# Optimization experiments

Hardware: AMD Instinct MI355X
Metric: run time of the kernel (lower is better)

Reference implementation:

```python
import jax, jax.numpy as jnp
import numpy as np

N_CORES = 64
N_QUBITS = 1024
QEMB = 256
N_EDGES = 448
BATCH = 512
NN_DIMS = (256, 512, 512, 256)


def setup_inputs() -> dict:
    key = jax.random.key(0)
    ks = jax.random.split(key, 12)
    inp = {
        "core_allocs": jax.random.randint(ks[0], (BATCH, N_QUBITS), 0, N_CORES, dtype=jnp.int32),
        "qubit_embs": jax.random.normal(ks[1], (N_QUBITS, QEMB), dtype=jnp.float32),
        "dummy_qubit_emb": jax.random.normal(ks[2], (QEMB,), dtype=jnp.float32),
        "edge_index": jax.random.randint(ks[3], (2, N_EDGES), 0, N_CORES, dtype=jnp.int32),
        "edge_weight": jax.random.uniform(ks[4], (N_EDGES,), dtype=jnp.float32),
        "W1": jax.random.normal(ks[5], (NN_DIMS[0], NN_DIMS[1]), dtype=jnp.float32) * 0.05,
        "b1": jax.random.normal(ks[6], (NN_DIMS[1],), dtype=jnp.float32) * 0.05,
        "W2": jax.random.normal(ks[7], (NN_DIMS[1], NN_DIMS[2]), dtype=jnp.float32) * 0.05,
        "b2": jax.random.normal(ks[8], (NN_DIMS[2],), dtype=jnp.float32) * 0.05,
        "W3": jax.random.normal(ks[9], (NN_DIMS[2], NN_DIMS[3]), dtype=jnp.float32) * 0.05,
        "b3": jax.random.normal(ks[10], (NN_DIMS[3],), dtype=jnp.float32) * 0.05,
    }
    return inp


def _gcn_norm(edge_index, edge_weight):
    # PyG gcn_norm: add self loops (weight 1), symmetric D^{-1/2} A D^{-1/2}.
    self_idx = jnp.arange(N_CORES, dtype=edge_index.dtype)
    row = jnp.concatenate([edge_index[0], self_idx])
    col = jnp.concatenate([edge_index[1], self_idx])
    w = jnp.concatenate([edge_weight, jnp.ones((N_CORES,), edge_weight.dtype)])
    deg = jax.ops.segment_sum(w, col, num_segments=N_CORES)  # degree at targets
    dinv = jnp.where(deg > 0, deg ** -0.5, 0.0)
    norm = dinv[row] * w * dinv[col]
    return row, col, norm


def reference(core_allocs, qubit_embs, dummy_qubit_emb, edge_index, edge_weight,
              W1, b1, W2, b2, W3, b3):
    # ---- unmixedCoreEmbs, vectorized: per-core max over assigned qubit embs,
    # dummy emb always included (cores never at capacity) ----
    def pool(alloc):  # alloc: [n_qubits] -> [n_cores, qemb]
        seg = jax.ops.segment_max(qubit_embs, alloc, num_segments=N_CORES)
        return jnp.maximum(seg, dummy_qubit_emb)  # also fixes -inf empty cores

    x = jax.vmap(pool)(core_allocs)  # [B, n_cores, qemb]

    # ---- GCNConv stack (same graph replicated per batch element) ----
    row, col, norm = _gcn_norm(edge_index, edge_weight)

    def gcn_layer(h, W, b):
        hw = h @ W  # [B, C, d_out]
        msg = hw[:, row, :] * norm[None, :, None]  # gather sources, scale
        agg = jnp.zeros((h.shape[0], N_CORES, W.shape[1]), hw.dtype).at[:, col, :].add(msg)
        return jax.nn.relu(agg + b)

    x = gcn_layer(x, W1, b1)
    x = gcn_layer(x, W2, b2)
    x = gcn_layer(x, W3, b3)
    return x  # [B, n_cores, nn_dims[-1]] (original returns this split per batch element)
```

## Files before the change

kernel.cpp:

```cpp
#include <hip/hip_runtime.h>
#include <type_traits>

typedef __attribute__((ext_vector_type(8))) short short8;
typedef __attribute__((ext_vector_type(4))) short short4v;
typedef __attribute__((ext_vector_type(4))) float f32x4;
typedef unsigned short u16;
typedef unsigned int u32;

#define N_EDGES 448

#define WS_ADJA 0
#define WS_ADJB 4096
#define WS_W1   8192
#define WS_W2   139264
#define WS_W3   401408
#define WS_DUM  532480
#define WS_B1   (WS_DUM + 256)
#define WS_B2   (WS_DUM + 768)
#define WS_B3   (WS_DUM + 1280)
#define WS_QE   534528

__device__ __forceinline__ float bf2f(u16 v) {
    u32 u = ((u32)v) << 16;
    return __builtin_bit_cast(float, u);
}
__device__ __forceinline__ u16 f2bf(float f) {
    u32 u = __builtin_bit_cast(u32, f);
    u32 r = u + 0x7FFFu + ((u >> 16) & 1u);
    return (u16)(r >> 16);
}
__device__ __forceinline__ float ldf(const void* p, int idx, u32 isf32) {
    return isf32 ? ((const float*)p)[idx] : bf2f(((const u16*)p)[idx]);
}

__global__ __launch_bounds__(512) void prep(
    const int* __restrict__ eidx, const void* __restrict__ ew,
    const void* __restrict__ qembs, const void* __restrict__ dummy,
    const void* __restrict__ W1, const void* __restrict__ b1,
    const void* __restrict__ W2, const void* __restrict__ b2,
    const void* __restrict__ W3, const void* __restrict__ b3,
    u16* __restrict__ ws) {
    const int t = threadIdx.x, bb = blockIdx.x;
    __shared__ u32 s_isf;
    if (t < 64) {
        const u16* qs = (const u16*)qembs;
        int c = 0;
#pragma unroll
        for (int j = 0; j < 4; j++) {
            u16 v = qs[(t * 4 + j) * 2];
            u32 e = (v >> 7) & 0xFF;
            c += (e >= 100 && e <= 134) ? 1 : 0;
        }
#pragma unroll
        for (int off = 32; off > 0; off >>= 1) c += __shfl_down(c, off, 64);
        if (t == 0) s_isf = (c < 128) ? 1u : 0u;
    }
    __syncthreads();
    const u32 isf32 = s_isf;

    if (t < 128) {
        const int bw = bb * 2 + (t >> 6);
        const int tl = t & 63;
        const void* src;
        int N, K32, dst, nt, kk;
        if (bw < 256)      { src = W1; N = 512; K32 = 8;  dst = WS_W1; nt = bw / 8;          kk = bw % 8; }
        else if (bw < 768) { src = W2; N = 512; K32 = 16; dst = WS_W2; nt = (bw - 256) / 16; kk = (bw - 256) % 16; }
        else               { src = W3; N = 256; K32 = 16; dst = WS_W3; nt = (bw - 768) / 16; kk = (bw - 768) % 16; }
        const int col = nt * 16 + (tl & 15);
        const int krow = kk * 32 + (tl >> 4) * 8;
        u16 v[8];
#pragma unroll
        for (int j = 0; j < 8; j++) v[j] = f2bf(ldf(src, (krow + j) * N + col, isf32));
        u16* o = ws + dst + (nt * K32 + kk) * 512 + tl * 8;
#pragma unroll
        for (int j = 0; j < 8; j++) o[j] = v[j];
    }
    if (t >= 256) {
        const int base = bb * 512 + (t - 256) * 2;
        ws[WS_QE + base]     = f2bf(ldf(qembs, base, isf32));
        ws[WS_QE + base + 1] = f2bf(ldf(qembs, base + 1, isf32));
    }
    if (bb == 1) {
#pragma unroll
        for (int j = 0; j < 4; j++) {
            int i = t + j * 512;
            if (i < 1792) {
                float v;
                if (i < 256)       v = ldf(dummy, i, isf32);
                else if (i < 768)  v = ldf(b1, i - 256, isf32);
                else if (i < 1280) v = ldf(b2, i - 768, isf32);
                else               v = ldf(b3, i - 1280, isf32);
                ws[WS_DUM + i] = f2bf(v);
            }
        }
    }
    if (bb == 0) {
        __shared__ float A[4096];
        __shared__ float deg[64];
        __shared__ float dinv[64];
        __shared__ int er[N_EDGES];
        __shared__ int ec[N_EDGES];
        __shared__ float ewf[N_EDGES];
        if (t < N_EDGES) {
            er[t] = eidx[t];
            ec[t] = eidx[N_EDGES + t];
            ewf[t] = ldf(ew, t, isf32);
        }
        if (t < 64) deg[t] = 1.0f;
        for (int i = t; i < 4096; i += 512) A[i] = 0.f;
        __syncthreads();
        if (t < N_EDGES) atomicAdd(&deg[ec[t]], ewf[t]);
        __syncthreads();
        if (t < 64) dinv[t] = 1.0f / sqrtf(deg[t]);
        __syncthreads();
        if (t < N_EDGES) atomicAdd(&A[ec[t] * 64 + er[t]], dinv[er[t]] * ewf[t] * dinv[ec[t]]);
        __syncthreads();
        if (t < 64) A[t * 64 + t] += dinv[t] * dinv[t];
        __syncthreads();
        for (int i = t; i < 4096; i += 512) {
            int chunk = i >> 9, m = (i >> 3) & 63, j = i & 7;
            ws[WS_ADJA + i] = f2bf(A[m * 64 + chunk * 8 + j]);
        }
        for (int i = t; i < 4096; i += 512) {
            int chunk = i >> 9, l = (i >> 3) & 63, j = i & 7;
            int ntc = chunk >> 1, kk = chunk & 1;
            int k = kk * 32 + (l >> 4) * 8 + j;
            int c2 = ntc * 16 + (l & 15);
            ws[WS_ADJB + i] = f2bf(A[c2 * 64 + k]);
        }
    }
}

__global__ __launch_bounds__(1024, 4) void fused(
    const int* __restrict__ allocs, const void* __restrict__ qembs,
    const u16* __restrict__ ws, void* __restrict__ out) {

    __shared__ __align__(16) u16 H[64 * 512];
    __shared__ u32 s_isf;

    const int t = threadIdx.x, bb = blockIdx.x;
    const int wave = t >> 6, lane = t & 63, quad = lane >> 4, nl = lane & 15;

    if (t < 64) {
        const u16* qs = (const u16*)qembs;
        int c = 0;
#pragma unroll
        for (int j = 0; j < 4; j++) {
            u16 v = qs[(t * 4 + j) * 2];
            u32 e = (v >> 7) & 0xFF;
            c += (e >= 100 && e <= 134) ? 1 : 0;
        }
#pragma unroll
        for (int off = 32; off > 0; off >>= 1) c += __shfl_down(c, off, 64);
        if (t == 0) s_isf = (c < 128) ? 1u : 0u;
    }
    __syncthreads();
    const u32 isf32 = s_isf;

    {
        int* LIST = (int*)H + 8192;
        int* CNT  = LIST + 1024;
        int* SST  = CNT + 64;
        int* WOF  = SST + 64;
        if (t < 64) CNT[t] = 0;
        __syncthreads();
        const int myc = allocs[bb * 1024 + t];
        atomicAdd(&CNT[myc], 1);
        __syncthreads();
        if (t < 64) {
            int v = CNT[t], s = v;
#pragma unroll
            for (int off = 1; off < 64; off <<= 1) {
                int u = __shfl_up(s, off, 64);
                if (t >= off) s += u;
            }
            SST[t] = s - v;
            WOF[t] = s - v;
        }
        __syncthreads();
        {
            int pos = atomicAdd(&WOF[myc], 1);
            LIST[pos] = t;
        }
        __syncthreads();
        float dums[4];
#pragma unroll
        for (int jj = 0; jj < 4; jj++) dums[jj] = bf2f(ws[WS_DUM + lane * 4 + jj]);
        const u16* wsq = ws + WS_QE;
        for (int i = 0; i < 4; i++) {
            const int c = wave * 4 + i;
            const int L = CNT[c], S = SST[c];
            float vm0 = -3.4e38f, vm1 = -3.4e38f, vm2 = -3.4e38f, vm3 = -3.4e38f;
            for (int j = 0; j < L; j++) {
                int q = LIST[S + j];
                uint2 r = *(const uint2*)(wsq + q * 256 + lane * 4);
                vm0 = fmaxf(vm0, bf2f((u16)(r.x & 0xffff)));
                vm1 = fmaxf(vm1, bf2f((u16)(r.x >> 16)));
                vm2 = fmaxf(vm2, bf2f((u16)(r.y & 0xffff)));
                vm3 = fmaxf(vm3, bf2f((u16)(r.y >> 16)));
            }
            short4v p;
            p[0] = (short)f2bf(fmaxf(vm0, dums[0]));
            p[1] = (short)f2bf(fmaxf(vm1, dums[1]));
            p[2] = (short)f2bf(fmaxf(vm2, dums[2]));
            p[3] = (short)f2bf(fmaxf(vm3, dums[3]));
            *(short4v*)(H + (lane >> 1) * 512 + c * 8 + (lane & 1) * 4) = p;
        }
    }
    __syncthreads();

    auto layerT = [&](auto K32c, const u16* __restrict__ W, const u16* __restrict__ bias) {
        constexpr int K32 = decltype(K32c)::value;
        const int s0 = wave * 2;
        u16* scr = H + (wave * 4 + 2) * 512;
        f32x4 acc[2][4];
#pragma unroll
        for (int s = 0; s < 2; s++)
#pragma unroll
            for (int rt = 0; rt < 4; rt++) acc[s][rt] = f32x4{0.f, 0.f, 0.f, 0.f};
#pragma unroll
        for (int kk = 0; kk < K32; kk++) {
            short8 a[4], bch[2];
#pragma unroll
            for (int rt = 0; rt < 4; rt++)
                a[rt] = *(const short8*)(H + (kk * 4 + quad) * 512 + (rt * 16 + nl) * 8);
#pragma unroll
            for (int s = 0; s < 2; s++)
                bch[s] = *(const short8*)(W + ((s0 + s) * K32 + kk) * 512 + lane * 8);
#pragma unroll
            for (int s = 0; s < 2; s++)
#pragma unroll
                for (int rt = 0; rt < 4; rt++)
                    acc[s][rt] = __builtin_amdgcn_mfma_f32_16x16x32_bf16(a[rt], bch[s], acc[s][rt], 0, 0, 0);
        }
        __syncthreads();
#pragma unroll
        for (int s = 0; s < 2; s++) {
            const int nt = s0 + s;
            f32x4 agg[4];
#pragma unroll
            for (int ntc = 0; ntc < 4; ntc++) agg[ntc] = f32x4{0.f, 0.f, 0.f, 0.f};
#pragma unroll
            for (int h = 0; h < 2; h++) {
#pragma unroll
                for (int r2 = 0; r2 < 2; r2++) {
                    f32x4 v = acc[s][2 * h + r2];
                    short4v p;
#pragma unroll
                    for (int rr = 0; rr < 4; rr++) p[rr] = (short)f2bf(v[rr]);
                    *(short4v*)(scr + nl * 40 + r2 * 16 + quad * 4) = p;
                }
                short8 hwf = *(const short8*)(scr + nl * 40 + quad * 8);
#pragma unroll
                for (int ntc = 0; ntc < 4; ntc++) {
                    short8 adjB = *(const short8*)(ws + WS_ADJB + (ntc * 2 + h) * 512 + lane * 8);
                    agg[ntc] = __builtin_amdgcn_mfma_f32_16x16x32_bf16(hwf, adjB, agg[ntc], 0, 0, 0);
                }
            }
            float bv[4];
#pragma unroll
            for (int rr = 0; rr < 4; rr++) bv[rr] = bf2f(bias[nt * 16 + quad * 4 + rr]);
#pragma unroll
            for (int ntc = 0; ntc < 4; ntc++) {
                short4v p;
#pragma unroll
                for (int rr = 0; rr < 4; rr++)
                    p[rr] = (short)f2bf(fmaxf(agg[ntc][rr] + bv[rr], 0.f));
                *(short4v*)(H + (nt * 2 + (quad >> 1)) * 512 + (ntc * 16 + nl) * 8 + (quad & 1) * 4) = p;
            }
        }
        __syncthreads();
    };

    auto layer3 = [&](const u16* __restrict__ W) {
        const int nt = wave;
        u16* scr = H + 16384 + wave * 640;
        f32x4 acc[4];
#pragma unroll
        for (int rt = 0; rt < 4; rt++) acc[rt] = f32x4{0.f, 0.f, 0.f, 0.f};
#pragma unroll
        for (int kk = 0; kk < 16; kk++) {
            short8 a[4];
#pragma unroll
            for (int rt = 0; rt < 4; rt++)
                a[rt] = *(const short8*)(H + (kk * 4 + quad) * 512 + (rt * 16 + nl) * 8);
            short8 bch = *(const short8*)(W + (nt * 16 + kk) * 512 + lane * 8);
#pragma unroll
            for (int rt = 0; rt < 4; rt++)
                acc[rt] = __builtin_amdgcn_mfma_f32_16x16x32_bf16(a[rt], bch, acc[rt], 0, 0, 0);
        }
        __syncthreads();
#pragma unroll
        for (int h = 0; h < 2; h++) {
#pragma unroll
            for (int r2 = 0; r2 < 2; r2++) {
                f32x4 v = acc[2 * h + r2];
                short4v p;
#pragma unroll
                for (int rr = 0; rr < 4; rr++) p[rr] = (short)f2bf(v[rr]);
                *(short4v*)(scr + nl * 40 + r2 * 16 + quad * 4) = p;
            }
            short8 hwf = *(const short8*)(scr + nl * 40 + quad * 8);
            *(short8*)(H + (nt * 2 + h) * 512 + lane * 8) = hwf;
        }
        __syncthreads();
    };

    auto finalOut = [&]() {
        const int rt2 = wave & 3, nt0 = (wave >> 2) * 4;
        short8 aA[2];
#pragma unroll
        for (int h = 0; h < 2; h++)
            aA[h] = *(const short8*)(ws + WS_ADJA + (h * 4 + quad) * 512 + (rt2 * 16 + nl) * 8);
        float* outf = (float*)out + (size_t)bb * 16384;
        u16* outu = (u16*)out + (size_t)bb * 16384;
#pragma unroll
        for (int ni = 0; ni < 4; ni++) {
            const int nt = nt0 + ni;
            short8 b0v = *(const short8*)(H + (nt * 2 + 0) * 512 + lane * 8);
            short8 b1v = *(const short8*)(H + (nt * 2 + 1) * 512 + lane * 8);
            f32x4 acc = f32x4{0.f, 0.f, 0.f, 0.f};
            acc = __builtin_amdgcn_mfma_f32_16x16x32_bf16(aA[0], b0v, acc, 0, 0, 0);
            acc = __builtin_amdgcn_mfma_f32_16x16x32_bf16(aA[1], b1v, acc, 0, 0, 0);
            const int n = nt * 16 + nl;
            const float bv = bf2f(ws[WS_B3 + n]);
#pragma unroll
            for (int rr = 0; rr < 4; rr++) {
                const int m2 = rt2 * 16 + quad * 4 + rr;
                float val = fmaxf(acc[rr] + bv, 0.f);
                if (isf32) outf[m2 * 256 + n] = val;
                else       outu[m2 * 256 + n] = f2bf(val);
            }
        }
    };

    layerT(std::integral_constant<int, 8>{},  ws + WS_W1, ws + WS_B1);
    layerT(std::integral_constant<int, 16>{}, ws + WS_W2, ws + WS_B2);
    layer3(ws + WS_W3);
    finalOut();
}

extern "C" void kernel_launch(void* const* d_in, const int* in_sizes, int n_in,
                              void* d_out, int out_size, void* d_ws, size_t ws_size,
                              hipStream_t stream) {
    const int* allocs = (const int*)d_in[0];
    const void* qembs = d_in[1];
    const void* dummy = d_in[2];
    const int* eidx   = (const int*)d_in[3];
    const void* ew    = d_in[4];
    const void* W1 = d_in[5];
    const void* b1 = d_in[6];
    const void* W2 = d_in[7];
    const void* b2 = d_in[8];
    const void* W3 = d_in[9];
    const void* b3 = d_in[10];
    u16* ws = (u16*)d_ws;

    prep<<<512, 512, 0, stream>>>(eidx, ew, qembs, dummy, W1, b1, W2, b2, W3, b3, ws);
    fused<<<512, 1024, 0, stream>>>(allocs, qembs, ws, d_out);
}
```

Before: 149.8 us.

## Stage final output through LDS for coalesced stores and widen pooling loads

```diff
diff --git a/kernel.cpp b/kernel.cpp
--- a/kernel.cpp
+++ b/kernel.cpp
@@ -19,6 +19,7 @@
 #define WS_B2   (WS_DUM + 768)
 #define WS_B3   (WS_DUM + 1280)
 #define WS_QE   534528
+#define WS_FLAG 796672
 
 __device__ __forceinline__ float bf2f(u16 v) {
     u32 u = ((u32)v) << 16;
@@ -128,34 +129,18 @@
             int c2 = ntc * 16 + (l & 15);
             ws[WS_ADJB + i] = f2bf(A[c2 * 64 + k]);
         }
-    }
-}
-
-__global__ __launch_bounds__(1024, 4) void fused(
-    const int* __restrict__ allocs, const void* __restrict__ qembs,
-    const u16* __restrict__ ws, void* __restrict__ out) {
+        if (t == 0) *(u32*)(ws + WS_FLAG) = isf32;
+    }
+}
+
+__global__ __launch_bounds__(1024, 8) void fused(
+    const int* __restrict__ allocs, const u16* __restrict__ ws,
+    void* __restrict__ out) {
 
     __shared__ __align__(16) u16 H[64 * 512];
-    __shared__ u32 s_isf;
 
     const int t = threadIdx.x, bb = blockIdx.x;
     const int wave = t >> 6, lane = t & 63, quad = lane >> 4, nl = lane & 15;
-
-    if (t < 64) {
-        const u16* qs = (const u16*)qembs;
-        int c = 0;
-#pragma unroll
-        for (int j = 0; j < 4; j++) {
-            u16 v = qs[(t * 4 + j) * 2];
-            u32 e = (v >> 7) & 0xFF;
-            c += (e >= 100 && e <= 134) ? 1 : 0;
-        }
-#pragma unroll
-        for (int off = 32; off > 0; off >>= 1) c += __shfl_down(c, off, 64);
-        if (t == 0) s_isf = (c < 128) ? 1u : 0u;
-    }
-    __syncthreads();
-    const u32 isf32 = s_isf;
 
     {
         int* LIST = (int*)H + 8192;
@@ -183,28 +168,33 @@
             LIST[pos] = t;
         }
         __syncthreads();
-        float dums[4];
-#pragma unroll
-        for (int jj = 0; jj < 4; jj++) dums[jj] = bf2f(ws[WS_DUM + lane * 4 + jj]);
+        const int half = lane >> 5, sl = lane & 31;
         const u16* wsq = ws + WS_QE;
         for (int i = 0; i < 4; i++) {
             const int c = wave * 4 + i;
             const int L = CNT[c], S = SST[c];
-            float vm0 = -3.4e38f, vm1 = -3.4e38f, vm2 = -3.4e38f, vm3 = -3.4e38f;
-            for (int j = 0; j < L; j++) {
+            float vm[8];
+#pragma unroll
+            for (int k = 0; k < 8; k++) vm[k] = bf2f(ws[WS_DUM + sl * 8 + k]);
+            for (int j = half; j < L; j += 2) {
                 int q = LIST[S + j];
-                uint2 r = *(const uint2*)(wsq + q * 256 + lane * 4);
-                vm0 = fmaxf(vm0, bf2f((u16)(r.x & 0xffff)));
-                vm1 = fmaxf(vm1, bf2f((u16)(r.x >> 16)));
-                vm2 = fmaxf(vm2, bf2f((u16)(r.y & 0xffff)));
-                vm3 = fmaxf(vm3, bf2f((u16)(r.y >> 16)));
-            }
-            short4v p;
-            p[0] = (short)f2bf(fmaxf(vm0, dums[0]));
-            p[1] = (short)f2bf(fmaxf(vm1, dums[1]));
-            p[2] = (short)f2bf(fmaxf(vm2, dums[2]));
-            p[3] = (short)f2bf(fmaxf(vm3, dums[3]));
-            *(short4v*)(H + (lane >> 1) * 512 + c * 8 + (lane & 1) * 4) = p;
+                uint4 r = *(const uint4*)(wsq + q * 256 + sl * 8);
+                vm[0] = fmaxf(vm[0], bf2f((u16)(r.x & 0xffff)));
+                vm[1] = fmaxf(vm[1], bf2f((u16)(r.x >> 16)));
+                vm[2] = fmaxf(vm[2], bf2f((u16)(r.y & 0xffff)));
+                vm[3] = fmaxf(vm[3], bf2f((u16)(r.y >> 16)));
+                vm[4] = fmaxf(vm[4], bf2f((u16)(r.z & 0xffff)));
+                vm[5] = fmaxf(vm[5], bf2f((u16)(r.z >> 16)));
+                vm[6] = fmaxf(vm[6], bf2f((u16)(r.w & 0xffff)));
+                vm[7] = fmaxf(vm[7], bf2f((u16)(r.w >> 16)));
+            }
+            short8 p;
+#pragma unroll
+            for (int k = 0; k < 8; k++) {
+                float o = __shfl_xor(vm[k], 32, 64);
+                p[k] = (short)f2bf(fmaxf(vm[k], o));
+            }
+            if (half == 0) *(short8*)(H + sl * 512 + c * 8) = p;
         }
     }
     __syncthreads();
@@ -307,29 +297,51 @@
     };
 
     auto finalOut = [&]() {
+        const u32 isf32 = *(const u32*)(ws + WS_FLAG);
         const int rt2 = wave & 3, nt0 = (wave >> 2) * 4;
         short8 aA[2];
 #pragma unroll
         for (int h = 0; h < 2; h++)
             aA[h] = *(const short8*)(ws + WS_ADJA + (h * 4 + quad) * 512 + (rt2 * 16 + nl) * 8);
-        float* outf = (float*)out + (size_t)bb * 16384;
-        u16* outu = (u16*)out + (size_t)bb * 16384;
+        f32x4 accv[4];
 #pragma unroll
         for (int ni = 0; ni < 4; ni++) {
             const int nt = nt0 + ni;
             short8 b0v = *(const short8*)(H + (nt * 2 + 0) * 512 + lane * 8);
             short8 b1v = *(const short8*)(H + (nt * 2 + 1) * 512 + lane * 8);
-            f32x4 acc = f32x4{0.f, 0.f, 0.f, 0.f};
-            acc = __builtin_amdgcn_mfma_f32_16x16x32_bf16(aA[0], b0v, acc, 0, 0, 0);
-            acc = __builtin_amdgcn_mfma_f32_16x16x32_bf16(aA[1], b1v, acc, 0, 0, 0);
-            const int n = nt * 16 + nl;
+            f32x4 a = f32x4{0.f, 0.f, 0.f, 0.f};
+            a = __builtin_amdgcn_mfma_f32_16x16x32_bf16(aA[0], b0v, a, 0, 0, 0);
+            a = __builtin_amdgcn_mfma_f32_16x16x32_bf16(aA[1], b1v, a, 0, 0, 0);
+            accv[ni] = a;
+        }
+        __syncthreads();
+        float* Hf = (float*)H;
+#pragma unroll
+        for (int ni = 0; ni < 4; ni++) {
+            const int n = (nt0 + ni) * 16 + nl;
             const float bv = bf2f(ws[WS_B3 + n]);
 #pragma unroll
             for (int rr = 0; rr < 4; rr++) {
                 const int m2 = rt2 * 16 + quad * 4 + rr;
-                float val = fmaxf(acc[rr] + bv, 0.f);
-                if (isf32) outf[m2 * 256 + n] = val;
-                else       outu[m2 * 256 + n] = f2bf(val);
+                Hf[m2 * 256 + n] = fmaxf(accv[ni][rr] + bv, 0.f);
+            }
+        }
+        __syncthreads();
+        if (isf32) {
+            float4* outv = (float4*)((float*)out + (size_t)bb * 16384);
+            const float4* Hv = (const float4*)Hf;
+#pragma unroll
+            for (int p4 = 0; p4 < 4; p4++) outv[p4 * 1024 + t] = Hv[p4 * 1024 + t];
+        } else {
+            u16* outu = (u16*)out + (size_t)bb * 16384;
+#pragma unroll
+            for (int p4 = 0; p4 < 4; p4++) {
+                const int idx = (p4 * 1024 + t) * 4;
+                float4 v = *(const float4*)(Hf + idx);
+                short4v pk;
+                pk[0] = (short)f2bf(v.x); pk[1] = (short)f2bf(v.y);
+                pk[2] = (short)f2bf(v.z); pk[3] = (short)f2bf(v.w);
+                *(short4v*)(outu + idx) = pk;
             }
         }
     };
@@ -357,5 +369,5 @@
     u16* ws = (u16*)d_ws;
 
     prep<<<512, 512, 0, stream>>>(eidx, ew, qembs, dummy, W1, b1, W2, b2, W3, b3, ws);
-    fused<<<512, 1024, 0, stream>>>(allocs, qembs, ws, d_out);
-}
+    fused<<<512, 1024, 0, stream>>>(allocs, ws, d_out);
+}
```

Measured after the change: 173.0 us. 1.15x slower.
